# Performance work log

Hardware: AMD Instinct MI355X
Metric: run time of the kernel (lower is better)

Reference implementation:

```python
import jax, jax.numpy as jnp
import numpy as np

N_NODES = 100000
N_EDGES = 1600000
D_IN = 128
D_OUT = 128


def setup_inputs() -> dict:
    key = jax.random.key(0)
    k1, k2, k3, k4 = jax.random.split(key, 4)
    feat = jax.random.normal(k1, (N_NODES, D_IN), dtype=jnp.float32)
    weight = jax.random.normal(k2, (D_IN, D_OUT), dtype=jnp.float32) * (1.0 / np.sqrt(D_IN))
    src = jax.random.randint(k3, (N_EDGES,), 0, N_NODES, dtype=jnp.int64)
    dst = jax.random.randint(k4, (N_EDGES,), 0, N_NODES, dtype=jnp.int64)
    return {"feat": feat, "weight": weight, "src": src, "dst": dst}


def reference(feat, weight, src, dst):
    n = feat.shape[0]
    ones = jnp.ones(src.shape[0], dtype=feat.dtype)
    # norm == 'both': scale source features by out_degree^{-1/2}
    out_deg = jnp.clip(jax.ops.segment_sum(ones, src, num_segments=n), 1.0)
    feat_src = feat * (out_deg ** -0.5)[:, None]  # [N, D_in]
    # update_all(copy_src, sum): gather src features, segment-sum into dst
    agg = jax.ops.segment_sum(feat_src[src], dst, num_segments=n)  # [N, D_in]
    # dense transform with external weight
    rst = agg @ weight  # [N, D_out]
    # destination-side normalization by in_degree^{-1/2}
    in_deg = jnp.clip(jax.ops.segment_sum(ones, dst, num_segments=n), 1.0)
    rst = rst * (in_deg ** -0.5)[:, None]
    return rst
```

## Files before the change

kernel.cpp:

```cpp
#include <hip/hip_runtime.h>
#include <stdint.h>


#define DIM 128
#define PN 128
#define MAXPP 800
#define CAPE 2560
#define CAPS 2560
#define PT 512
#define EPT 13
#define CHUNK (PT * EPT)
#define CAPA 1536

typedef unsigned int uint;
typedef unsigned short ushortT;

__device__ __forceinline__ ushortT f2bf(float x) {
    uint u = __float_as_uint(x);
    u = (u + 0x7FFFu + ((u >> 16) & 1u)) >> 16;
    return (ushortT)u;
}
__device__ __forceinline__ float bf2f(ushortT b) {
    return __uint_as_float(((uint)b) << 16);
}

__global__ __launch_bounds__(PT) void part(
    const int* __restrict__ src, const int* __restrict__ dst,
    int* __restrict__ curD, int* __restrict__ curS,
    int* __restrict__ pairs, unsigned char* __restrict__ srcb,
    int E, int NPP) {
    __shared__ int cD[MAXPP], cS[MAXPP];
    __shared__ int lofD[MAXPP], lofS[MAXPP];
    __shared__ int gbD[MAXPP], gbS[MAXPP];
    __shared__ int bufD[CHUNK];
    __shared__ unsigned char bufS[CHUNK];

    int tid = threadIdx.x;
    long long base = (long long)blockIdx.x * CHUNK;
    for (int i = tid; i < NPP; i += PT) { cD[i] = 0; cS[i] = 0; }
    __syncthreads();

    int sv[EPT], dv[EPT], lrD[EPT], lrS[EPT];
#pragma unroll
    for (int j = 0; j < EPT; ++j) {
        long long e = base + tid + j * PT;
        bool ok = e < E;
        int s = 0, d = 0;
        if (ok) { s = src[e]; d = dst[e]; }
        sv[j] = s; dv[j] = d;
        lrD[j] = ok ? atomicAdd(&cD[d >> 7], 1) : 0;
        lrS[j] = ok ? atomicAdd(&cS[s >> 7], 1) : 0;
    }
    __syncthreads();

    int* sc = bufD;
    for (int pass = 0; pass < 2; ++pass) {
        const int* cnts = pass ? cS : cD;
        int* lof = pass ? lofS : lofD;
        for (int i = tid; i < 1024; i += PT) sc[i] = (i < NPP) ? cnts[i] : 0;
        __syncthreads();
        for (int off = 1; off < 1024; off <<= 1) {
            int i0 = tid, i1 = tid + PT;
            int a0 = (i0 >= off) ? sc[i0 - off] : 0;
            int a1 = (i1 >= off) ? sc[i1 - off] : 0;
            __syncthreads();
            sc[i0] += a0; sc[i1] += a1;
            __syncthreads();
        }
        for (int i = tid; i < NPP; i += PT) lof[i] = sc[i] - cnts[i];
        __syncthreads();
    }

    for (int i = tid; i < NPP; i += PT) {
        int c = cD[i];
        gbD[i] = c ? atomicAdd(&curD[i], c) : 0;
        c = cS[i];
        gbS[i] = c ? atomicAdd(&curS[i], c) : 0;
    }

#pragma unroll
    for (int j = 0; j < EPT; ++j) {
        long long e = base + tid + j * PT;
        if (e < E) {
            int s = sv[j], d = dv[j];
            bufD[lofD[d >> 7] + lrD[j]] = (s << 7) | (d & 127);
            bufS[lofS[s >> 7] + lrS[j]] = (unsigned char)(s & 127);
        }
    }
    __syncthreads();

    int cnt = (int)(((long long)E - base < (long long)CHUNK) ? (E - base) : CHUNK);
    for (int i = tid; i < cnt; i += PT) {
        int lo = 0, hi = NPP - 1;
        while (lo < hi) { int mid = (lo + hi + 1) >> 1; if (lofD[mid] <= i) lo = mid; else hi = mid - 1; }
        int pos = gbD[lo] + (i - lofD[lo]);
        if (pos < CAPE) pairs[(size_t)lo * CAPE + pos] = bufD[i];
    }
    for (int i = tid; i < cnt; i += PT) {
        int lo = 0, hi = NPP - 1;
        while (lo < hi) { int mid = (lo + hi + 1) >> 1; if (lofS[mid] <= i) lo = mid; else hi = mid - 1; }
        int pos = gbS[lo] + (i - lofS[lo]);
        if (pos < CAPS) srcb[(size_t)lo * CAPS + pos] = bufS[i];
    }
}

__global__ __launch_bounds__(256) void deg(
    const int* __restrict__ curS, const unsigned char* __restrict__ srcb,
    float* __restrict__ oscale, int N) {
    __shared__ int hist[PN];
    int p = blockIdx.x, tid = threadIdx.x;
    if (tid < PN) hist[tid] = 0;
    __syncthreads();
    int cnt = min(curS[p], CAPS);
    const unsigned char* b = &srcb[(size_t)p * CAPS];
    for (int i = tid; i < cnt; i += 256) atomicAdd(&hist[b[i]], 1);
    __syncthreads();
    if (tid < PN) {
        int node = p * PN + tid;
        if (node < N) oscale[node] = rsqrtf((float)max(hist[tid], 1));
    }
}

__global__ __launch_bounds__(256) void gemm_h(
    const float* __restrict__ feat, const float* __restrict__ W,
    const float* __restrict__ oscale, ushortT* __restrict__ h, int M) {
    __shared__ float As[32][36];
    __shared__ float Bs[32][128];

    int tid = threadIdx.x;
    int m0 = blockIdx.x * 32;
    int tx = tid & 31;
    int ty = tid >> 5;
    int bc = tx << 2;

    float acc[4][4];
#pragma unroll
    for (int r = 0; r < 4; ++r)
#pragma unroll
        for (int c = 0; c < 4; ++c) acc[r][c] = 0.f;

    int am = tid >> 3;
    int ak = (tid & 7) << 2;
    int arow = m0 + am;
    float scale = (arow < M) ? oscale[arow] : 0.f;

    for (int k0 = 0; k0 < DIM; k0 += 32) {
        float4 a = make_float4(0.f, 0.f, 0.f, 0.f);
        if (arow < M) a = *(const float4*)&feat[(size_t)arow * DIM + k0 + ak];
        As[ak + 0][am] = a.x * scale;
        As[ak + 1][am] = a.y * scale;
        As[ak + 2][am] = a.z * scale;
        As[ak + 3][am] = a.w * scale;
#pragma unroll
        for (int i = 0; i < 4; ++i) {
            int k = ty + i * 8;
            *(float4*)&Bs[k][bc] = *(const float4*)&W[(size_t)(k0 + k) * DIM + bc];
        }
        __syncthreads();
#pragma unroll
        for (int k = 0; k < 32; ++k) {
            float4 a4 = *(const float4*)&As[k][ty << 2];
            float4 b4 = *(const float4*)&Bs[k][bc];
            acc[0][0] += a4.x * b4.x; acc[0][1] += a4.x * b4.y; acc[0][2] += a4.x * b4.z; acc[0][3] += a4.x * b4.w;
            acc[1][0] += a4.y * b4.x; acc[1][1] += a4.y * b4.y; acc[1][2] += a4.y * b4.z; acc[1][3] += a4.y * b4.w;
            acc[2][0] += a4.z * b4.x; acc[2][1] += a4.z * b4.y; acc[2][2] += a4.z * b4.z; acc[2][3] += a4.z * b4.w;
            acc[3][0] += a4.w * b4.x; acc[3][1] += a4.w * b4.y; acc[3][2] += a4.w * b4.z; acc[3][3] += a4.w * b4.w;
        }
        __syncthreads();
    }
    float* T = &Bs[0][0];
#pragma unroll
    for (int r = 0; r < 4; ++r)
#pragma unroll
        for (int j = 0; j < 4; ++j)
            T[((ty << 2) + r) * 128 + bc + j] = acc[r][j];
    __syncthreads();
    for (int q = tid; q < 1024; q += 256) {
        int row = q >> 5, l = q & 31;
        int m = m0 + row;
        if (m < M) {
            ushort4 v;
            v.x = f2bf(T[row * 128 + l]);
            v.y = f2bf(T[row * 128 + l + 32]);
            v.z = f2bf(T[row * 128 + l + 64]);
            v.w = f2bf(T[row * 128 + l + 96]);
            *(ushort4*)&h[(size_t)m * DIM + (l << 2)] = v;
        }
    }
}

__global__ __launch_bounds__(256) void aggp(
    const ushortT* __restrict__ h, const int* __restrict__ pairs,
    const int* __restrict__ curD, float* __restrict__ out, int N) {
    __shared__ int sorted[CAPA];
    __shared__ int hist[64], offs[64], cur[64];
    int b = blockIdx.x;
    int p = b >> 1, sub = b & 1;
    int tid = threadIdx.x;
    if (tid < 64) hist[tid] = 0;
    __syncthreads();
    int cnt = min(curD[p], CAPE);
    const int* pb = &pairs[(size_t)p * CAPE];
    for (int i = tid; i < cnt; i += 256) {
        int dl = pb[i] & 127;
        if ((dl >> 6) == sub) atomicAdd(&hist[dl & 63], 1);
    }
    __syncthreads();
    if (tid < 64) {
        int x = hist[tid], incl = x;
        for (int o = 1; o < 64; o <<= 1) {
            int y = __shfl_up(incl, o, 64);
            if (tid >= o) incl += y;
        }
        offs[tid] = incl - x;
        cur[tid] = incl - x;
    }
    __syncthreads();
    for (int i = tid; i < cnt; i += 256) {
        int w = pb[i];
        int dl = w & 127;
        if ((dl >> 6) == sub) {
            int slot = atomicAdd(&cur[dl & 63], 1);
            if (slot < CAPA) sorted[slot] = w >> 7;
        }
    }
    __syncthreads();
    int hw = tid >> 5, l = tid & 31;
    for (int nd = hw; nd < 64; nd += 8) {
        int node = p * PN + sub * 64 + nd;
        if (node >= N) continue;
        int start = offs[nd];
        int degn = hist[nd];
        int end = min(start + degn, CAPA);
        float a0 = 0.f, a1 = 0.f, a2 = 0.f, a3 = 0.f;
        int e = start;
        for (; e + 8 <= end; e += 8) {
            int s0 = sorted[e],     s1 = sorted[e + 1];
            int s2 = sorted[e + 2], s3 = sorted[e + 3];
            int s4 = sorted[e + 4], s5 = sorted[e + 5];
            int s6 = sorted[e + 6], s7 = sorted[e + 7];
            ushort4 v0 = *(const ushort4*)&h[(size_t)s0 * DIM + (l << 2)];
            ushort4 v1 = *(const ushort4*)&h[(size_t)s1 * DIM + (l << 2)];
            ushort4 v2 = *(const ushort4*)&h[(size_t)s2 * DIM + (l << 2)];
            ushort4 v3 = *(const ushort4*)&h[(size_t)s3 * DIM + (l << 2)];
            ushort4 v4 = *(const ushort4*)&h[(size_t)s4 * DIM + (l << 2)];
            ushort4 v5 = *(const ushort4*)&h[(size_t)s5 * DIM + (l << 2)];
            ushort4 v6 = *(const ushort4*)&h[(size_t)s6 * DIM + (l << 2)];
            ushort4 v7 = *(const ushort4*)&h[(size_t)s7 * DIM + (l << 2)];
            a0 += ((bf2f(v0.x) + bf2f(v1.x)) + (bf2f(v2.x) + bf2f(v3.x))) +
                  ((bf2f(v4.x) + bf2f(v5.x)) + (bf2f(v6.x) + bf2f(v7.x)));
            a1 += ((bf2f(v0.y) + bf2f(v1.y)) + (bf2f(v2.y) + bf2f(v3.y))) +
                  ((bf2f(v4.y) + bf2f(v5.y)) + (bf2f(v6.y) + bf2f(v7.y)));
            a2 += ((bf2f(v0.z) + bf2f(v1.z)) + (bf2f(v2.z) + bf2f(v3.z))) +
                  ((bf2f(v4.z) + bf2f(v5.z)) + (bf2f(v6.z) + bf2f(v7.z)));
            a3 += ((bf2f(v0.w) + bf2f(v1.w)) + (bf2f(v2.w) + bf2f(v3.w))) +
                  ((bf2f(v4.w) + bf2f(v5.w)) + (bf2f(v6.w) + bf2f(v7.w)));
        }
        for (; e < end; ++e) {
            int s0 = sorted[e];
            ushort4 v0 = *(const ushort4*)&h[(size_t)s0 * DIM + (l << 2)];
            a0 += bf2f(v0.x); a1 += bf2f(v0.y);
            a2 += bf2f(v0.z); a3 += bf2f(v0.w);
        }
        float scn = rsqrtf((float)max(degn, 1));
        size_t ob = (size_t)node * DIM;
        out[ob + l]      = a0 * scn;
        out[ob + l + 32] = a1 * scn;
        out[ob + l + 64] = a2 * scn;
        out[ob + l + 96] = a3 * scn;
    }
}

extern "C" void kernel_launch(void* const* d_in, const int* in_sizes, int n_in,
                              void* d_out, int out_size, void* d_ws, size_t ws_size,
                              hipStream_t stream) {
    const float* feat = (const float*)d_in[0];
    const float* W    = (const float*)d_in[1];
    const int*   src  = (const int*)d_in[2];
    const int*   dst  = (const int*)d_in[3];
    float* out = (float*)d_out;

    int N = in_sizes[0] / DIM;
    int E = in_sizes[2];
    int NPP = (N + PN - 1) / PN;

    int* curD = (int*)d_ws;
    int* curS = curD + NPP;
    float* oscale = (float*)(curS + NPP);
    int* pairs = (int*)(oscale + N);
    unsigned char* srcb = (unsigned char*)(pairs + (size_t)NPP * CAPE);
    uintptr_t hp = (uintptr_t)(srcb + (size_t)NPP * CAPS);
    ushortT* h = (ushortT*)((hp + 15) & ~(uintptr_t)15);

    hipMemsetAsync(curD, 0, (size_t)2 * NPP * sizeof(int), stream);

    int nb = (E + CHUNK - 1) / CHUNK;
    part<<<nb, PT, 0, stream>>>(src, dst, curD, curS, pairs, srcb, E, NPP);
    deg<<<NPP, 256, 0, stream>>>(curS, srcb, oscale, N);
    gemm_h<<<(N + 31) / 32, 256, 0, stream>>>(feat, W, oscale, h, N);
    aggp<<<2 * NPP, 256, 0, stream>>>(h, pairs, curD, out, N);
}
```

Measured before the change: 274.1 us.

## Rework partition scan, scatter, GEMM epilogue and aggregation block mapping

In the partition kernel, the block-wide Hillis-Steele scan is replaced by two single-wave shuffle scans, and the per-element binary search in the scatter step is replaced by per-partition copy loops, one wave per partition. The GEMM epilogue now writes bf16 straight from registers and no longer stages the tile through shared memory. Aggregation uses one 512-thread block per 128-node partition instead of two 256-thread half-blocks, so the edge list is read once rather than twice. Each wave handles one node and each lane does 4-byte gathers, trading wider per-lane loads and shorter unrolling for coalesced float2 stores.

```diff
diff --git a/kernel.cpp b/kernel.cpp
--- a/kernel.cpp
+++ b/kernel.cpp
@@ -10,7 +10,6 @@
 #define PT 512
 #define EPT 13
 #define CHUNK (PT * EPT)
-#define CAPA 1536
 
 typedef unsigned int uint;
 typedef unsigned short ushortT;
@@ -19,9 +18,6 @@
     uint u = __float_as_uint(x);
     u = (u + 0x7FFFu + ((u >> 16) & 1u)) >> 16;
     return (ushortT)u;
-}
-__device__ __forceinline__ float bf2f(ushortT b) {
-    return __uint_as_float(((uint)b) << 16);
 }
 
 __global__ __launch_bounds__(PT) void part(
@@ -36,6 +32,7 @@
     __shared__ unsigned char bufS[CHUNK];
 
     int tid = threadIdx.x;
+    int wv = tid >> 6, l = tid & 63;
     long long base = (long long)blockIdx.x * CHUNK;
     for (int i = tid; i < NPP; i += PT) { cD[i] = 0; cS[i] = 0; }
     __syncthreads();
@@ -53,23 +50,23 @@
     }
     __syncthreads();
 
-    int* sc = bufD;
-    for (int pass = 0; pass < 2; ++pass) {
-        const int* cnts = pass ? cS : cD;
-        int* lof = pass ? lofS : lofD;
-        for (int i = tid; i < 1024; i += PT) sc[i] = (i < NPP) ? cnts[i] : 0;
-        __syncthreads();
-        for (int off = 1; off < 1024; off <<= 1) {
-            int i0 = tid, i1 = tid + PT;
-            int a0 = (i0 >= off) ? sc[i0 - off] : 0;
-            int a1 = (i1 >= off) ? sc[i1 - off] : 0;
-            __syncthreads();
-            sc[i0] += a0; sc[i1] += a1;
-            __syncthreads();
-        }
-        for (int i = tid; i < NPP; i += PT) lof[i] = sc[i] - cnts[i];
-        __syncthreads();
-    }
+    if (wv < 2) {
+        const int* cnts = wv ? cS : cD;
+        int* lof = wv ? lofS : lofD;
+        int carry = 0;
+        for (int b = 0; b < NPP; b += 64) {
+            int i = b + l;
+            int x = (i < NPP) ? cnts[i] : 0;
+            int incl = x;
+            for (int o = 1; o < 64; o <<= 1) {
+                int y = __shfl_up(incl, o, 64);
+                if (l >= o) incl += y;
+            }
+            if (i < NPP) lof[i] = carry + incl - x;
+            carry += __shfl(incl, 63, 64);
+        }
+    }
+    __syncthreads();
 
     for (int i = tid; i < NPP; i += PT) {
         int c = cD[i];
@@ -89,18 +86,13 @@
     }
     __syncthreads();
 
-    int cnt = (int)(((long long)E - base < (long long)CHUNK) ? (E - base) : CHUNK);
-    for (int i = tid; i < cnt; i += PT) {
-        int lo = 0, hi = NPP - 1;
-        while (lo < hi) { int mid = (lo + hi + 1) >> 1; if (lofD[mid] <= i) lo = mid; else hi = mid - 1; }
-        int pos = gbD[lo] + (i - lofD[lo]);
-        if (pos < CAPE) pairs[(size_t)lo * CAPE + pos] = bufD[i];
-    }
-    for (int i = tid; i < cnt; i += PT) {
-        int lo = 0, hi = NPP - 1;
-        while (lo < hi) { int mid = (lo + hi + 1) >> 1; if (lofS[mid] <= i) lo = mid; else hi = mid - 1; }
-        int pos = gbS[lo] + (i - lofS[lo]);
-        if (pos < CAPS) srcb[(size_t)lo * CAPS + pos] = bufS[i];
+    for (int pp = wv; pp < NPP; pp += 8) {
+        int lo = lofD[pp], len = cD[pp], gb = gbD[pp];
+        for (int j = l; j < len; j += 64)
+            if (gb + j < CAPE) pairs[(size_t)pp * CAPE + gb + j] = bufD[lo + j];
+        lo = lofS[pp]; len = cS[pp]; gb = gbS[pp];
+        for (int j = l; j < len; j += 64)
+            if (gb + j < CAPS) srcb[(size_t)pp * CAPS + gb + j] = bufS[lo + j];
     }
 }
 
@@ -168,106 +160,82 @@
         }
         __syncthreads();
     }
-    float* T = &Bs[0][0];
-#pragma unroll
-    for (int r = 0; r < 4; ++r)
-#pragma unroll
-        for (int j = 0; j < 4; ++j)
-            T[((ty << 2) + r) * 128 + bc + j] = acc[r][j];
-    __syncthreads();
-    for (int q = tid; q < 1024; q += 256) {
-        int row = q >> 5, l = q & 31;
-        int m = m0 + row;
+#pragma unroll
+    for (int r = 0; r < 4; ++r) {
+        int m = m0 + (ty << 2) + r;
         if (m < M) {
             ushort4 v;
-            v.x = f2bf(T[row * 128 + l]);
-            v.y = f2bf(T[row * 128 + l + 32]);
-            v.z = f2bf(T[row * 128 + l + 64]);
-            v.w = f2bf(T[row * 128 + l + 96]);
-            *(ushort4*)&h[(size_t)m * DIM + (l << 2)] = v;
-        }
-    }
-}
-
-__global__ __launch_bounds__(256) void aggp(
+            v.x = f2bf(acc[r][0]);
+            v.y = f2bf(acc[r][1]);
+            v.z = f2bf(acc[r][2]);
+            v.w = f2bf(acc[r][3]);
+            *(ushort4*)&h[(size_t)m * DIM + bc] = v;
+        }
+    }
+}
+
+__global__ __launch_bounds__(PT) void aggp(
     const ushortT* __restrict__ h, const int* __restrict__ pairs,
     const int* __restrict__ curD, float* __restrict__ out, int N) {
-    __shared__ int sorted[CAPA];
-    __shared__ int hist[64], offs[64], cur[64];
-    int b = blockIdx.x;
-    int p = b >> 1, sub = b & 1;
-    int tid = threadIdx.x;
-    if (tid < 64) hist[tid] = 0;
+    __shared__ int sorted[CAPE];
+    __shared__ int hist[PN], offs[PN], cur[PN];
+    int p = blockIdx.x, tid = threadIdx.x;
+    int wv = tid >> 6, l = tid & 63;
+    if (tid < PN) hist[tid] = 0;
     __syncthreads();
     int cnt = min(curD[p], CAPE);
     const int* pb = &pairs[(size_t)p * CAPE];
-    for (int i = tid; i < cnt; i += 256) {
-        int dl = pb[i] & 127;
-        if ((dl >> 6) == sub) atomicAdd(&hist[dl & 63], 1);
-    }
+    for (int i = tid; i < cnt; i += PT) atomicAdd(&hist[pb[i] & 127], 1);
     __syncthreads();
     if (tid < 64) {
-        int x = hist[tid], incl = x;
+        int i0 = tid << 1;
+        int x0 = hist[i0], x1 = hist[i0 + 1];
+        int pairsum = x0 + x1;
+        int incl = pairsum;
         for (int o = 1; o < 64; o <<= 1) {
             int y = __shfl_up(incl, o, 64);
             if (tid >= o) incl += y;
         }
-        offs[tid] = incl - x;
-        cur[tid] = incl - x;
-    }
-    __syncthreads();
-    for (int i = tid; i < cnt; i += 256) {
+        int excl = incl - pairsum;
+        offs[i0] = excl;     offs[i0 + 1] = excl + x0;
+        cur[i0]  = excl;     cur[i0 + 1]  = excl + x0;
+    }
+    __syncthreads();
+    for (int i = tid; i < cnt; i += PT) {
         int w = pb[i];
-        int dl = w & 127;
-        if ((dl >> 6) == sub) {
-            int slot = atomicAdd(&cur[dl & 63], 1);
-            if (slot < CAPA) sorted[slot] = w >> 7;
-        }
-    }
-    __syncthreads();
-    int hw = tid >> 5, l = tid & 31;
-    for (int nd = hw; nd < 64; nd += 8) {
-        int node = p * PN + sub * 64 + nd;
+        int slot = atomicAdd(&cur[w & 127], 1);
+        if (slot < CAPE) sorted[slot] = w >> 7;
+    }
+    __syncthreads();
+    for (int nd = wv; nd < PN; nd += 8) {
+        int node = p * PN + nd;
         if (node >= N) continue;
         int start = offs[nd];
         int degn = hist[nd];
-        int end = min(start + degn, CAPA);
-        float a0 = 0.f, a1 = 0.f, a2 = 0.f, a3 = 0.f;
+        int end = min(start + degn, CAPE);
+        float a0 = 0.f, a1 = 0.f;
         int e = start;
-        for (; e + 8 <= end; e += 8) {
+        for (; e + 4 <= end; e += 4) {
             int s0 = sorted[e],     s1 = sorted[e + 1];
             int s2 = sorted[e + 2], s3 = sorted[e + 3];
-            int s4 = sorted[e + 4], s5 = sorted[e + 5];
-            int s6 = sorted[e + 6], s7 = sorted[e + 7];
-            ushort4 v0 = *(const ushort4*)&h[(size_t)s0 * DIM + (l << 2)];
-            ushort4 v1 = *(const ushort4*)&h[(size_t)s1 * DIM + (l << 2)];
-            ushort4 v2 = *(const ushort4*)&h[(size_t)s2 * DIM + (l << 2)];
-            ushort4 v3 = *(const ushort4*)&h[(size_t)s3 * DIM + (l << 2)];
-            ushort4 v4 = *(const ushort4*)&h[(size_t)s4 * DIM + (l << 2)];
-            ushort4 v5 = *(const ushort4*)&h[(size_t)s5 * DIM + (l << 2)];
-            ushort4 v6 = *(const ushort4*)&h[(size_t)s6 * DIM + (l << 2)];
-            ushort4 v7 = *(const ushort4*)&h[(size_t)s7 * DIM + (l << 2)];
-            a0 += ((bf2f(v0.x) + bf2f(v1.x)) + (bf2f(v2.x) + bf2f(v3.x))) +
-                  ((bf2f(v4.x) + bf2f(v5.x)) + (bf2f(v6.x) + bf2f(v7.x)));
-            a1 += ((bf2f(v0.y) + bf2f(v1.y)) + (bf2f(v2.y) + bf2f(v3.y))) +
-                  ((bf2f(v4.y) + bf2f(v5.y)) + (bf2f(v6.y) + bf2f(v7.y)));
-            a2 += ((bf2f(v0.z) + bf2f(v1.z)) + (bf2f(v2.z) + bf2f(v3.z))) +
-                  ((bf2f(v4.z) + bf2f(v5.z)) + (bf2f(v6.z) + bf2f(v7.z)));
-            a3 += ((bf2f(v0.w) + bf2f(v1.w)) + (bf2f(v2.w) + bf2f(v3.w))) +
-                  ((bf2f(v4.w) + bf2f(v5.w)) + (bf2f(v6.w) + bf2f(v7.w)));
+            uint u0 = *(const uint*)&h[(size_t)s0 * DIM + (l << 1)];
+            uint u1 = *(const uint*)&h[(size_t)s1 * DIM + (l << 1)];
+            uint u2 = *(const uint*)&h[(size_t)s2 * DIM + (l << 1)];
+            uint u3 = *(const uint*)&h[(size_t)s3 * DIM + (l << 1)];
+            a0 += (__uint_as_float(u0 << 16) + __uint_as_float(u1 << 16)) +
+                  (__uint_as_float(u2 << 16) + __uint_as_float(u3 << 16));
+            a1 += (__uint_as_float(u0 & 0xffff0000u) + __uint_as_float(u1 & 0xffff0000u)) +
+                  (__uint_as_float(u2 & 0xffff0000u) + __uint_as_float(u3 & 0xffff0000u));
         }
         for (; e < end; ++e) {
             int s0 = sorted[e];
-            ushort4 v0 = *(const ushort4*)&h[(size_t)s0 * DIM + (l << 2)];
-            a0 += bf2f(v0.x); a1 += bf2f(v0.y);
-            a2 += bf2f(v0.z); a3 += bf2f(v0.w);
-        }
-        float scn = rsqrtf((float)max(degn, 1));
-        size_t ob = (size_t)node * DIM;
-        out[ob + l]      = a0 * scn;
-        out[ob + l + 32] = a1 * scn;
-        out[ob + l + 64] = a2 * scn;
-        out[ob + l + 96] = a3 * scn;
+            uint u0 = *(const uint*)&h[(size_t)s0 * DIM + (l << 1)];
+            a0 += __uint_as_float(u0 << 16);
+            a1 += __uint_as_float(u0 & 0xffff0000u);
+        }
+        float sc = rsqrtf((float)max(degn, 1));
+        *(float2*)&out[(size_t)node * DIM + (l << 1)] =
+            make_float2(a0 * sc, a1 * sc);
     }
 }
 
@@ -298,5 +266,5 @@
     part<<<nb, PT, 0, stream>>>(src, dst, curD, curS, pairs, srcb, E, NPP);
     deg<<<NPP, 256, 0, stream>>>(curS, srcb, oscale, N);
     gemm_h<<<(N + 31) / 32, 256, 0, stream>>>(feat, W, oscale, h, N);
-    aggp<<<2 * NPP, 256, 0, stream>>>(h, pairs, curD, out, N);
-}
+    aggp<<<NPP, PT, 0, stream>>>(h, pairs, curD, out, N);
+}
```

Result: slower. 290.7 us (+6.1%).
